# Kernel tuning notes

Measured on AMD Instinct MI355X. Metric: run time of the kernel, lower is better.

## Reference

```python
import jax, jax.numpy as jnp
import numpy as np

CLIP_LIMIT = 2.0
TILES_Y, TILES_X = 8, 8
NUM_BINS = 256


def setup_inputs() -> dict:
    key = jax.random.key(0)
    image = jax.random.uniform(key, (32, 1, 1024, 1024), dtype=jnp.float32)
    return {"image": image}


def reference(image) -> jnp.ndarray:
    B, C, H, W = image.shape
    th, tw = H // TILES_Y, W // TILES_X
    n_tiles = B * TILES_Y * TILES_X

    img = image[:, 0]  # (B, H, W); original only processes channel 0
    # Split into tiles: (B, Ty, th, Tx, tw) -> (n_tiles, th*tw)
    tiles = img.reshape(B, TILES_Y, th, TILES_X, tw)
    tiles = tiles.transpose(0, 1, 3, 2, 4).reshape(n_tiles, th * tw)

    # torch.histc(bins=256, min=0, max=1): bin = floor(x*256), clipped to [0,255]
    hist_bin = jnp.clip((tiles * NUM_BINS).astype(jnp.int32), 0, NUM_BINS - 1)
    seg_ids = (jnp.arange(n_tiles, dtype=jnp.int32)[:, None] * NUM_BINS + hist_bin).ravel()
    hist = jax.ops.segment_sum(
        jnp.ones(tiles.size, dtype=jnp.float32), seg_ids,
        num_segments=n_tiles * NUM_BINS).reshape(n_tiles, NUM_BINS)

    # Clip and redistribute excess uniformly
    clip_count = hist.sum(axis=-1, keepdims=True) * CLIP_LIMIT / NUM_BINS
    excess = jnp.maximum(hist - clip_count, 0.0).sum(axis=-1, keepdims=True)
    hist_c = jnp.minimum(hist, clip_count) + excess / NUM_BINS

    cdf = jnp.cumsum(hist_c, axis=-1)
    cdf = cdf / cdf[:, -1:]

    # Gather uses floor(x*255) indexing (as in the original, differs from histc binning)
    idx = jnp.clip((tiles * (NUM_BINS - 1)).astype(jnp.int32), 0, NUM_BINS - 1)
    mapped = jnp.take_along_axis(cdf, idx, axis=1)  # (n_tiles, th*tw)

    out = mapped.reshape(B, TILES_Y, TILES_X, th, tw).transpose(0, 1, 3, 2, 4)
    out = out.reshape(B, TILES_Y * th, TILES_X * tw)
    return out[:, None, :, :]  # (B, 1, H, W)
```

## Files before the change

### kernel.cpp

```cpp
#include <hip/hip_runtime.h>

#define IMG_W 1024
#define IMG_H 1024

typedef float f32x4 __attribute__((ext_vector_type(4)));

__global__ __launch_bounds__(256, 4) void clahe_kernel(const float* __restrict__ img,
                                                       float* __restrict__ out) {
    const int pair = blockIdx.x;
    const int tA = pair << 1;
    const int b  = tA >> 6;
    const int ty = (tA >> 3) & 7;
    const int tx = tA & 7;

    const size_t baseA = ((size_t)b * IMG_H + (size_t)ty * 128) * IMG_W + (size_t)tx * 128;
    const size_t baseB = baseA + 128;

    const int t = threadIdx.x;
    const int w = t >> 6;

    __shared__ int   hist[4][256];
    __shared__ float cdf[2][256];
    __shared__ float exw[4];
    __shared__ float wsum[4];

    const size_t toff = (size_t)(t >> 5) * IMG_W + ((t & 31) << 2);
    const float* __restrict__ pA = img + baseA + toff;
    const float* __restrict__ pB = img + baseB + toff;
    float* __restrict__ dA = out + baseA + toff;
    float* __restrict__ dB = out + baseB + toff;

    hist[0][t] = 0; hist[1][t] = 0; hist[2][t] = 0; hist[3][t] = 0;
    __syncthreads();

    unsigned int pkA[16], pkB[16];
    f32x4 va[8], vb[8];

    auto binpack = [&](const f32x4 v, unsigned int* pk) {
        atomicAdd(&hist[w][min(255, (int)(v.x * 256.0f))], 1);
        atomicAdd(&hist[w][min(255, (int)(v.y * 256.0f))], 1);
        atomicAdd(&hist[w][min(255, (int)(v.z * 256.0f))], 1);
        atomicAdd(&hist[w][min(255, (int)(v.w * 256.0f))], 1);
        *pk = (unsigned int)min(255, (int)(v.x * 255.0f))
            | ((unsigned int)min(255, (int)(v.y * 255.0f)) << 8)
            | ((unsigned int)min(255, (int)(v.z * 255.0f)) << 16)
            | ((unsigned int)min(255, (int)(v.w * 255.0f)) << 24);
    };

    auto scan_fn = [&](int s) {
        const int h = hist[0][t] + hist[1][t] + hist[2][t] + hist[3][t];
        hist[0][t] = 0; hist[1][t] = 0; hist[2][t] = 0; hist[3][t] = 0;

        float ex = (float)max(h - 128, 0);
        #pragma unroll
        for (int off = 32; off > 0; off >>= 1) ex += __shfl_xor(ex, off);
        if ((t & 63) == 0) exw[w] = ex;

        float x = fminf((float)h, 128.0f);
        #pragma unroll
        for (int off = 1; off < 64; off <<= 1) {
            const float y = __shfl_up(x, off);
            if ((t & 63) >= off) x += y;
        }
        if ((t & 63) == 63) wsum[w] = x;
        __syncthreads();

        const float excess = exw[0] + exw[1] + exw[2] + exw[3];
        float prefix = 0.0f;
        if (w > 0) prefix += wsum[0];
        if (w > 1) prefix += wsum[1];
        if (w > 2) prefix += wsum[2];
        const float summinh = wsum[0] + wsum[1] + wsum[2] + wsum[3];
        const float e256 = excess * (1.0f / 256.0f);
        const float total = summinh + excess;
        cdf[s][t] = (x + prefix + (float)(t + 1) * e256) / total;
    };

    #pragma unroll
    for (int j = 0; j < 8; ++j)
        va[j] = *reinterpret_cast<const f32x4*>(pA + (size_t)j * 8 * IMG_W);
    #pragma unroll
    for (int j = 0; j < 8; ++j)
        vb[j] = *reinterpret_cast<const f32x4*>(pA + (size_t)(j + 8) * 8 * IMG_W);
    #pragma unroll
    for (int j = 0; j < 8; ++j) binpack(va[j], &pkA[j]);
    #pragma unroll
    for (int j = 0; j < 8; ++j)
        va[j] = *reinterpret_cast<const f32x4*>(pB + (size_t)j * 8 * IMG_W);
    #pragma unroll
    for (int j = 0; j < 8; ++j) binpack(vb[j], &pkA[j + 8]);
    __syncthreads();

    scan_fn(0);
    __syncthreads();

    #pragma unroll
    for (int j = 0; j < 8; ++j)
        vb[j] = *reinterpret_cast<const f32x4*>(pB + (size_t)(j + 8) * 8 * IMG_W);
    #pragma unroll
    for (int j = 0; j < 8; ++j) {
        binpack(va[j], &pkB[j]);
        const unsigned int u = pkA[j];
        f32x4 o;
        o.x = cdf[0][u & 255u];
        o.y = cdf[0][(u >> 8) & 255u];
        o.z = cdf[0][(u >> 16) & 255u];
        o.w = cdf[0][u >> 24];
        __builtin_nontemporal_store(
            o, reinterpret_cast<f32x4*>(dA + (size_t)j * 8 * IMG_W));
    }
    #pragma unroll
    for (int j = 0; j < 8; ++j) {
        binpack(vb[j], &pkB[j + 8]);
        const unsigned int u = pkA[j + 8];
        f32x4 o;
        o.x = cdf[0][u & 255u];
        o.y = cdf[0][(u >> 8) & 255u];
        o.z = cdf[0][(u >> 16) & 255u];
        o.w = cdf[0][u >> 24];
        __builtin_nontemporal_store(
            o, reinterpret_cast<f32x4*>(dA + (size_t)(j + 8) * 8 * IMG_W));
    }
    __syncthreads();

    scan_fn(1);
    __syncthreads();

    #pragma unroll
    for (int i = 0; i < 16; ++i) {
        const unsigned int u = pkB[i];
        f32x4 o;
        o.x = cdf[1][u & 255u];
        o.y = cdf[1][(u >> 8) & 255u];
        o.z = cdf[1][(u >> 16) & 255u];
        o.w = cdf[1][u >> 24];
        __builtin_nontemporal_store(
            o, reinterpret_cast<f32x4*>(dB + (size_t)i * 8 * IMG_W));
    }
}

extern "C" void kernel_launch(void* const* d_in, const int* in_sizes, int n_in,
                              void* d_out, int out_size, void* d_ws, size_t ws_size,
                              hipStream_t stream) {
    const float* img = (const float*)d_in[0];
    float* out = (float*)d_out;
    clahe_kernel<<<1024, 256, 0, stream>>>(img, out);
}
```

Baseline: 51.63 us.

## Process four tiles per 512-thread block with a rolling histogram/map pipeline

Each block now handles four horizontally adjacent tiles instead of two, using 512 threads. The block loops over the tiles, loading the next tile and writing the previous tile's mapped output while it builds the current histogram, with double-buffered CDFs. Only 256 threads do the scan, and eight per-wave histograms are merged. The aim is to raise per-block parallelism and overlap loads, stores and scans across tiles. The cost is fewer blocks (512), more barriers per block, and idle threads during each scan.

Measured after the change: 44.22 us, median of 2. 14.4% less time.

```diff
diff --git a/kernel.cpp b/kernel.cpp
--- a/kernel.cpp
+++ b/kernel.cpp
@@ -5,137 +5,124 @@
 
 typedef float f32x4 __attribute__((ext_vector_type(4)));
 
-__global__ __launch_bounds__(256, 4) void clahe_kernel(const float* __restrict__ img,
+__global__ __launch_bounds__(512, 4) void clahe_kernel(const float* __restrict__ img,
                                                        float* __restrict__ out) {
-    const int pair = blockIdx.x;
-    const int tA = pair << 1;
-    const int b  = tA >> 6;
-    const int ty = (tA >> 3) & 7;
-    const int tx = tA & 7;
+    const int quad = blockIdx.x;
+    const int t0 = quad << 2;
+    const int b  = t0 >> 6;
+    const int ty = (t0 >> 3) & 7;
+    const int tx = t0 & 7;
 
-    const size_t baseA = ((size_t)b * IMG_H + (size_t)ty * 128) * IMG_W + (size_t)tx * 128;
-    const size_t baseB = baseA + 128;
+    const size_t base0 = ((size_t)b * IMG_H + (size_t)ty * 128) * IMG_W + (size_t)tx * 128;
 
     const int t = threadIdx.x;
     const int w = t >> 6;
 
-    __shared__ int   hist[4][256];
+    __shared__ int   hist[8][256];
     __shared__ float cdf[2][256];
     __shared__ float exw[4];
     __shared__ float wsum[4];
 
-    const size_t toff = (size_t)(t >> 5) * IMG_W + ((t & 31) << 2);
-    const float* __restrict__ pA = img + baseA + toff;
-    const float* __restrict__ pB = img + baseB + toff;
-    float* __restrict__ dA = out + baseA + toff;
-    float* __restrict__ dB = out + baseB + toff;
-
-    hist[0][t] = 0; hist[1][t] = 0; hist[2][t] = 0; hist[3][t] = 0;
+    int* hflat = &hist[0][0];
+    hflat[t] = 0; hflat[t + 512] = 0; hflat[t + 1024] = 0; hflat[t + 1536] = 0;
     __syncthreads();
 
-    unsigned int pkA[16], pkB[16];
-    f32x4 va[8], vb[8];
+    const size_t toff = (size_t)(t >> 5) * IMG_W + ((t & 31) << 2);
+    const float* __restrict__ p0 = img + base0 + toff;
+    float* __restrict__ d0 = out + base0 + toff;
 
-    auto binpack = [&](const f32x4 v, unsigned int* pk) {
-        atomicAdd(&hist[w][min(255, (int)(v.x * 256.0f))], 1);
-        atomicAdd(&hist[w][min(255, (int)(v.y * 256.0f))], 1);
-        atomicAdd(&hist[w][min(255, (int)(v.z * 256.0f))], 1);
-        atomicAdd(&hist[w][min(255, (int)(v.w * 256.0f))], 1);
-        *pk = (unsigned int)min(255, (int)(v.x * 255.0f))
-            | ((unsigned int)min(255, (int)(v.y * 255.0f)) << 8)
-            | ((unsigned int)min(255, (int)(v.z * 255.0f)) << 16)
-            | ((unsigned int)min(255, (int)(v.w * 255.0f)) << 24);
+    unsigned int pk[2][8];
+    f32x4 v[8];
+
+    auto binpack = [&](const f32x4 vv, unsigned int* pkp) {
+        atomicAdd(&hist[w][min(255, (int)(vv.x * 256.0f))], 1);
+        atomicAdd(&hist[w][min(255, (int)(vv.y * 256.0f))], 1);
+        atomicAdd(&hist[w][min(255, (int)(vv.z * 256.0f))], 1);
+        atomicAdd(&hist[w][min(255, (int)(vv.w * 256.0f))], 1);
+        *pkp = (unsigned int)min(255, (int)(vv.x * 255.0f))
+             | ((unsigned int)min(255, (int)(vv.y * 255.0f)) << 8)
+             | ((unsigned int)min(255, (int)(vv.z * 255.0f)) << 16)
+             | ((unsigned int)min(255, (int)(vv.w * 255.0f)) << 24);
     };
 
     auto scan_fn = [&](int s) {
-        const int h = hist[0][t] + hist[1][t] + hist[2][t] + hist[3][t];
-        hist[0][t] = 0; hist[1][t] = 0; hist[2][t] = 0; hist[3][t] = 0;
+        int h = 0;
+        float x = 0.0f;
+        if (t < 256) {
+            h = hist[0][t] + hist[1][t] + hist[2][t] + hist[3][t]
+              + hist[4][t] + hist[5][t] + hist[6][t] + hist[7][t];
 
-        float ex = (float)max(h - 128, 0);
-        #pragma unroll
-        for (int off = 32; off > 0; off >>= 1) ex += __shfl_xor(ex, off);
-        if ((t & 63) == 0) exw[w] = ex;
+            float ex = (float)max(h - 128, 0);
+            #pragma unroll
+            for (int off = 32; off > 0; off >>= 1) ex += __shfl_xor(ex, off);
+            if ((t & 63) == 0) exw[w] = ex;
 
-        float x = fminf((float)h, 128.0f);
-        #pragma unroll
-        for (int off = 1; off < 64; off <<= 1) {
-            const float y = __shfl_up(x, off);
-            if ((t & 63) >= off) x += y;
+            x = fminf((float)h, 128.0f);
+            #pragma unroll
+            for (int off = 1; off < 64; off <<= 1) {
+                const float y = __shfl_up(x, off);
+                if ((t & 63) >= off) x += y;
+            }
+            if ((t & 63) == 63) wsum[w] = x;
         }
-        if ((t & 63) == 63) wsum[w] = x;
         __syncthreads();
-
-        const float excess = exw[0] + exw[1] + exw[2] + exw[3];
-        float prefix = 0.0f;
-        if (w > 0) prefix += wsum[0];
-        if (w > 1) prefix += wsum[1];
-        if (w > 2) prefix += wsum[2];
-        const float summinh = wsum[0] + wsum[1] + wsum[2] + wsum[3];
-        const float e256 = excess * (1.0f / 256.0f);
-        const float total = summinh + excess;
-        cdf[s][t] = (x + prefix + (float)(t + 1) * e256) / total;
+        hflat[t] = 0; hflat[t + 512] = 0; hflat[t + 1024] = 0; hflat[t + 1536] = 0;
+        if (t < 256) {
+            const float excess = exw[0] + exw[1] + exw[2] + exw[3];
+            float prefix = 0.0f;
+            if (w > 0) prefix += wsum[0];
+            if (w > 1) prefix += wsum[1];
+            if (w > 2) prefix += wsum[2];
+            const float summinh = wsum[0] + wsum[1] + wsum[2] + wsum[3];
+            const float e256 = excess * (1.0f / 256.0f);
+            const float total = summinh + excess;
+            cdf[s][t] = (x + prefix + (float)(t + 1) * e256) / total;
+        }
     };
 
     #pragma unroll
-    for (int j = 0; j < 8; ++j)
-        va[j] = *reinterpret_cast<const f32x4*>(pA + (size_t)j * 8 * IMG_W);
-    #pragma unroll
-    for (int j = 0; j < 8; ++j)
-        vb[j] = *reinterpret_cast<const f32x4*>(pA + (size_t)(j + 8) * 8 * IMG_W);
-    #pragma unroll
-    for (int j = 0; j < 8; ++j) binpack(va[j], &pkA[j]);
-    #pragma unroll
-    for (int j = 0; j < 8; ++j)
-        va[j] = *reinterpret_cast<const f32x4*>(pB + (size_t)j * 8 * IMG_W);
-    #pragma unroll
-    for (int j = 0; j < 8; ++j) binpack(vb[j], &pkA[j + 8]);
-    __syncthreads();
+    for (int i = 0; i < 4; ++i) {
+        const float* pi = p0 + (size_t)i * 128;
+        #pragma unroll
+        for (int j = 0; j < 8; ++j)
+            v[j] = *reinterpret_cast<const f32x4*>(pi + (size_t)j * 16 * IMG_W);
 
-    scan_fn(0);
-    __syncthreads();
+        if (i > 0) {
+            float* dprev = d0 + (size_t)(i - 1) * 128;
+            #pragma unroll
+            for (int j = 0; j < 8; ++j) {
+                const unsigned int u = pk[(i - 1) & 1][j];
+                f32x4 o;
+                o.x = cdf[(i - 1) & 1][u & 255u];
+                o.y = cdf[(i - 1) & 1][(u >> 8) & 255u];
+                o.z = cdf[(i - 1) & 1][(u >> 16) & 255u];
+                o.w = cdf[(i - 1) & 1][u >> 24];
+                __builtin_nontemporal_store(
+                    o, reinterpret_cast<f32x4*>(dprev + (size_t)j * 16 * IMG_W));
+            }
+        }
 
-    #pragma unroll
-    for (int j = 0; j < 8; ++j)
-        vb[j] = *reinterpret_cast<const f32x4*>(pB + (size_t)(j + 8) * 8 * IMG_W);
-    #pragma unroll
-    for (int j = 0; j < 8; ++j) {
-        binpack(va[j], &pkB[j]);
-        const unsigned int u = pkA[j];
-        f32x4 o;
-        o.x = cdf[0][u & 255u];
-        o.y = cdf[0][(u >> 8) & 255u];
-        o.z = cdf[0][(u >> 16) & 255u];
-        o.w = cdf[0][u >> 24];
-        __builtin_nontemporal_store(
-            o, reinterpret_cast<f32x4*>(dA + (size_t)j * 8 * IMG_W));
+        #pragma unroll
+        for (int j = 0; j < 8; ++j) binpack(v[j], &pk[i & 1][j]);
+        __syncthreads();
+
+        scan_fn(i & 1);
+        __syncthreads();
     }
-    #pragma unroll
-    for (int j = 0; j < 8; ++j) {
-        binpack(vb[j], &pkB[j + 8]);
-        const unsigned int u = pkA[j + 8];
-        f32x4 o;
-        o.x = cdf[0][u & 255u];
-        o.y = cdf[0][(u >> 8) & 255u];
-        o.z = cdf[0][(u >> 16) & 255u];
-        o.w = cdf[0][u >> 24];
-        __builtin_nontemporal_store(
-            o, reinterpret_cast<f32x4*>(dA + (size_t)(j + 8) * 8 * IMG_W));
-    }
-    __syncthreads();
 
-    scan_fn(1);
-    __syncthreads();
-
-    #pragma unroll
-    for (int i = 0; i < 16; ++i) {
-        const unsigned int u = pkB[i];
-        f32x4 o;
-        o.x = cdf[1][u & 255u];
-        o.y = cdf[1][(u >> 8) & 255u];
-        o.z = cdf[1][(u >> 16) & 255u];
-        o.w = cdf[1][u >> 24];
-        __builtin_nontemporal_store(
-            o, reinterpret_cast<f32x4*>(dB + (size_t)i * 8 * IMG_W));
+    {
+        float* dprev = d0 + (size_t)3 * 128;
+        #pragma unroll
+        for (int j = 0; j < 8; ++j) {
+            const unsigned int u = pk[1][j];
+            f32x4 o;
+            o.x = cdf[1][u & 255u];
+            o.y = cdf[1][(u >> 8) & 255u];
+            o.z = cdf[1][(u >> 16) & 255u];
+            o.w = cdf[1][u >> 24];
+            __builtin_nontemporal_store(
+                o, reinterpret_cast<f32x4*>(dprev + (size_t)j * 16 * IMG_W));
+        }
     }
 }
 
@@ -144,5 +131,5 @@
                               hipStream_t stream) {
     const float* img = (const float*)d_in[0];
     float* out = (float*)d_out;
-    clahe_kernel<<<1024, 256, 0, stream>>>(img, out);
+    clahe_kernel<<<512, 512, 0, stream>>>(img, out);
 }
```
